# Kernel optimization log

Measured on AMD Instinct MI355X. Metric: run time of the kernel, lower is better.

The kernel has to match this reference:

```python
import jax, jax.numpy as jnp
import numpy as np

N = 50000      # nodes
E = 800000     # edges
IN = 256       # in_dim
HID = 64       # num_hidden
H0 = 4         # heads[0]
H1 = 1         # heads[1]
OUT1 = HID * H0  # 256, last GATConv out_feats
C = 64         # num_classes
NEG_SLOPE = 0.2


def setup_inputs() -> dict:
    ks = jax.random.split(jax.random.key(0), 13)
    s = 0.05
    return {
        "x":   jax.random.normal(ks[0], (N, IN), jnp.float32),
        "src": jax.random.randint(ks[1], (E,), 0, N, jnp.int32),
        "dst": jax.random.randint(ks[2], (E,), 0, N, jnp.int32),
        # layer 0: GATConv(IN, HID, H0)
        "W0":  jax.random.normal(ks[3], (IN, H0 * HID), jnp.float32) * s,
        "al0": jax.random.normal(ks[4], (H0, HID), jnp.float32) * s,
        "ar0": jax.random.normal(ks[5], (H0, HID), jnp.float32) * s,
        "b0":  jnp.zeros((H0 * HID,), jnp.float32),
        # layer 1: GATConv(H0*HID, OUT1, H1), residual (identity since in == H1*OUT1)
        "W1":  jax.random.normal(ks[6], (H0 * HID, H1 * OUT1), jnp.float32) * s,
        "al1": jax.random.normal(ks[7], (H1, OUT1), jnp.float32) * s,
        "ar1": jax.random.normal(ks[8], (H1, OUT1), jnp.float32) * s,
        "b1":  jnp.zeros((H1 * OUT1,), jnp.float32),
        # final classifier Linear(OUT1, C)
        "Wl":  jax.random.normal(ks[9], (OUT1, C), jnp.float32) * s,
        "bl":  jnp.zeros((C,), jnp.float32),
    }


def gat_conv(h, src, dst, W, al, ar, b, heads, out, residual, act):
    # ft: projected per-head features [N, H, D]
    ft = (h @ W).reshape(-1, heads, out)
    el = jnp.sum(ft * al, axis=-1)          # [N, H]
    er = jnp.sum(ft * ar, axis=-1)          # [N, H]
    e = jax.nn.leaky_relu(el[src] + er[dst], NEG_SLOPE)  # [E, H]
    # edge softmax grouped by destination node
    emax = jax.ops.segment_max(e, dst, num_segments=N)
    a = jnp.exp(e - emax[dst])
    asum = jax.ops.segment_sum(a, dst, num_segments=N)
    alpha = a / asum[dst]                   # [E, H]
    msg = alpha[:, :, None] * ft[src]       # [E, H, D]
    rst = jax.ops.segment_sum(msg, dst, num_segments=N)  # [N, H, D]
    if residual:  # identity residual (in_feats == heads*out)
        rst = rst + h.reshape(-1, heads, out)
    rst = rst + b.reshape(1, heads, out)
    if act is not None:
        rst = act(rst)
    return rst


def reference(x, src, dst, W0, al0, ar0, b0, W1, al1, ar1, b1, Wl, bl):
    h = gat_conv(x, src, dst, W0, al0, ar0, b0, H0, HID, False, jax.nn.elu)
    h = h.reshape(N, -1)                    # flatten(1) -> [N, H0*HID]
    h = gat_conv(h, src, dst, W1, al1, ar1, b1, H1, OUT1, True, None)
    h = h.mean(axis=1)                      # mean over heads -> [N, OUT1]
    logits = h @ Wl + bl
    return (logits, h)
```

## Files before the change

### kernel.cpp

```cpp
#include <hip/hip_runtime.h>
#include <hip/hip_bf16.h>
#include <stdint.h>

#define NNODES 50000
#define NEDGES 800000
#define CH     256
#define NCLS   64
#define DCAP   64

typedef __attribute__((ext_vector_type(8))) short  short8;
typedef __attribute__((ext_vector_type(4))) float  floatx4;

__device__ __forceinline__ float bf2f(unsigned short u) {
    union { unsigned int i; float f; } v; v.i = ((unsigned int)u) << 16; return v.f;
}
__device__ __forceinline__ unsigned short f2bf(float f) {
    union { float f; unsigned int i; } v; v.f = f;
    unsigned int x = v.i;
    return (unsigned short)((x + 0x7fffu + ((x >> 16) & 1u)) >> 16);
}

__device__ __forceinline__ void gl_lds16(const void* g, void* l) {
    __builtin_amdgcn_global_load_lds(
        (const __attribute__((address_space(1))) unsigned int*)g,
        (__attribute__((address_space(3))) unsigned int*)l, 16, 0, 0);
}

__global__ void k_setup(const float* __restrict__ W0, const float* __restrict__ W1,
                        const float* __restrict__ Wl, const float* __restrict__ x,
                        unsigned short* __restrict__ w0t, unsigned short* __restrict__ w1t,
                        unsigned short* __restrict__ wlt, unsigned short* __restrict__ xbf,
                        int* __restrict__ cnt) {
    int i = blockIdx.x * 256 + threadIdx.x;
    if (i < 65536) {
        int r = i >> 8, c = i & 255;
        w0t[c * 256 + r] = f2bf(W0[i]);
    } else if (i < 131072) {
        int j = i - 65536;
        int r = j >> 8, c = j & 255;
        w1t[c * 256 + r] = f2bf(W1[j]);
    } else if (i < 147456) {
        int j = i - 131072;
        int r = j >> 6, c = j & 63;
        wlt[c * 256 + r] = f2bf(Wl[j]);
    } else if (i < 147456 + NNODES) {
        cnt[i - 147456] = 0;
    } else {
        int j = i - (147456 + NNODES);
        if (j < NNODES * CH / 8) {
            const float4* xp = (const float4*)(x + (size_t)j * 8);
            float4 v0 = xp[0], v1 = xp[1];
            ushort4 o0, o1;
            o0.x = f2bf(v0.x); o0.y = f2bf(v0.y); o0.z = f2bf(v0.z); o0.w = f2bf(v0.w);
            o1.x = f2bf(v1.x); o1.y = f2bf(v1.y); o1.z = f2bf(v1.z); o1.w = f2bf(v1.w);
            *(ushort4*)(xbf + (size_t)j * 8)     = o0;
            *(ushort4*)(xbf + (size_t)j * 8 + 4) = o1;
        }
    }
}

__global__ void k_scatter(const int* __restrict__ dst, const int* __restrict__ src,
                          int* __restrict__ cnt, int* __restrict__ esrc) {
    int e = blockIdx.x * 256 + threadIdx.x;
    if (e < NEDGES) {
        int d = dst[e];
        if ((unsigned)d < NNODES) {
            int p = atomicAdd(&cnt[d], 1);
            if (p < DCAP) esrc[(size_t)d * DCAP + p] = src[e];
        }
    }
}

template<int BN, bool AF32, bool OUTF32, int HEL>
__global__ __launch_bounds__(256) void k_gemml(const void* __restrict__ Av,
                                               const unsigned short* __restrict__ BT,
                                               const float* __restrict__ bias,
                                               float* __restrict__ Cf,
                                               unsigned short* __restrict__ Cb,
                                               int M, int N,
                                               const float* __restrict__ al,
                                               const float* __restrict__ ar,
                                               float* __restrict__ el,
                                               float* __restrict__ er) {
    constexpr int NT  = BN / 16;
    constexpr int RPW = BN / 4;
    constexpr int P   = RPW / 16;
    __shared__ unsigned short Bs[2][BN][32];
    const int t  = threadIdx.x;
    const int w  = t >> 6, l = t & 63;
    const int lm = l & 15, lg = l >> 4;
    const int m0 = blockIdx.x * 64;
    const int arow = m0 + w * 16 + lm;
    const unsigned short* Ab = (const unsigned short*)Av;
    const float*          Af = (const float*)Av;

    const int srow  = w * RPW + (l >> 2);
    const int sslot = (l & 3) * 8;

    floatx4 acc[NT];
#pragma unroll
    for (int nt = 0; nt < NT; ++nt) acc[nt] = (floatx4)0.0f;

#pragma unroll
    for (int p = 0; p < P; ++p)
        gl_lds16(BT + (size_t)(srow + p * 16) * 256 + sslot,
                 &Bs[0][w * RPW + p * 16][0]);
    short8 af0 = (short8)0, af1 = (short8)0;
    if (arow < M) {
        if (AF32) {
            const float* ap = Af + (size_t)arow * 256 + lg * 8;
            float4 v0 = *(const float4*)(ap), v1 = *(const float4*)(ap + 4);
            af0[0] = (short)f2bf(v0.x); af0[1] = (short)f2bf(v0.y);
            af0[2] = (short)f2bf(v0.z); af0[3] = (short)f2bf(v0.w);
            af0[4] = (short)f2bf(v1.x); af0[5] = (short)f2bf(v1.y);
            af0[6] = (short)f2bf(v1.z); af0[7] = (short)f2bf(v1.w);
        } else {
            af0 = *(const short8*)(Ab + (size_t)arow * 256 + lg * 8);
        }
    }
    __syncthreads();

    int cur = 0;
    for (int ks = 0; ks < 8; ++ks) {
        if (ks < 7) {
            int k1 = (ks + 1) * 32;
#pragma unroll
            for (int p = 0; p < P; ++p)
                gl_lds16(BT + (size_t)(srow + p * 16) * 256 + k1 + sslot,
                         &Bs[cur ^ 1][w * RPW + p * 16][0]);
            af1 = (short8)0;
            if (arow < M) {
                if (AF32) {
                    const float* ap = Af + (size_t)arow * 256 + k1 + lg * 8;
                    float4 v0 = *(const float4*)(ap), v1 = *(const float4*)(ap + 4);
                    af1[0] = (short)f2bf(v0.x); af1[1] = (short)f2bf(v0.y);
                    af1[2] = (short)f2bf(v0.z); af1[3] = (short)f2bf(v0.w);
                    af1[4] = (short)f2bf(v1.x); af1[5] = (short)f2bf(v1.y);
                    af1[6] = (short)f2bf(v1.z); af1[7] = (short)f2bf(v1.w);
                } else {
                    af1 = *(const short8*)(Ab + (size_t)arow * 256 + k1 + lg * 8);
                }
            }
        }
#pragma unroll
        for (int nt = 0; nt < NT; ++nt) {
            short8 bf = *(const short8*)&Bs[cur][nt * 16 + lm][lg * 8];
            acc[nt] = __builtin_amdgcn_mfma_f32_16x16x32_bf16(af0, bf, acc[nt], 0, 0, 0);
        }
        af0 = af1;
        if (ks < 7) { __syncthreads(); cur ^= 1; }
    }

    float alv[HEL > 0 ? NT : 1], arv[HEL > 0 ? NT : 1];
    if (HEL > 0) {
#pragma unroll
        for (int nt = 0; nt < NT; ++nt) {
            alv[nt] = al[nt * 16 + lm];
            arv[nt] = ar[nt * 16 + lm];
        }
    }

#pragma unroll
    for (int j = 0; j < 4; ++j) {
        int row = m0 + w * 16 + (l >> 4) * 4 + j;
        if (row < M) {
#pragma unroll
            for (int nt = 0; nt < NT; ++nt) {
                int gcol = nt * 16 + lm;
                float v = acc[nt][j];
                if (bias) v += bias[gcol];
                if (OUTF32) Cf[(size_t)row * N + gcol] = v;
                else        Cb[(size_t)row * N + gcol] = f2bf(v);
            }
            if (HEL > 0) {
#pragma unroll
                for (int h = 0; h < HEL; ++h) {
                    float sl = 0.f, sr = 0.f;
#pragma unroll
                    for (int q = 0; q < NT / HEL; ++q) {
                        int nt = h * (NT / HEL) + q;
                        float v = acc[nt][j];
                        sl += v * alv[nt];
                        sr += v * arv[nt];
                    }
#pragma unroll
                    for (int mm = 1; mm < 16; mm <<= 1) {
                        sl += __shfl_xor(sl, mm, 64);
                        sr += __shfl_xor(sr, mm, 64);
                    }
                    if (lm == 0) {
                        el[(size_t)row * HEL + h] = sl;
                        er[(size_t)row * HEL + h] = sr;
                    }
                }
            }
        }
    }
}

template<int H, bool ELU, bool RESID>
__global__ __launch_bounds__(256) void k_agg5(
        const unsigned short* __restrict__ ft,
        const float* __restrict__ el, const float* __restrict__ er,
        const int* __restrict__ cnt,
        const int* __restrict__ esrc,
        const unsigned short* __restrict__ resid16,
        const float* __restrict__ bias,
        unsigned short* __restrict__ out_bf,
        float* __restrict__ out_f) {
    int w = threadIdx.x >> 6;
    int n = blockIdx.x * 4 + w;
    int l = threadIdx.x & 63;
    int c = 4 * l;
    int st = n * DCAP;
    int dg = __builtin_amdgcn_readfirstlane(cnt[n]);
    if (dg > DCAP) dg = DCAP;
    if (dg < 0) dg = 0;
    float a0 = 0.f, a1 = 0.f, a2 = 0.f, a3 = 0.f, wsum = 0.f;
    const unsigned short* ftc = ft + c;

    if (H == 1) {
        float ern = er[n];
        for (int i = 0; i < dg; i += 64) {
            int idx = i + l;
            int sv = 0; float wv = 0.f;
            if (idx < dg) {
                sv = esrc[st + idx];
                float xv = el[sv] + ern;
                xv = (xv > 0.f) ? xv : 0.2f * xv;
                xv = fminf(xv, 60.f);
                wv = __expf(xv);
            }
            wsum += wv;
            int jmax = dg - i; if (jmax > 64) jmax = 64;
            int j = 0;
            for (; j + 4 <= jmax; j += 4) {
                int s0 = __builtin_amdgcn_readlane(sv, j + 0);
                int s1 = __builtin_amdgcn_readlane(sv, j + 1);
                int s2 = __builtin_amdgcn_readlane(sv, j + 2);
                int s3 = __builtin_amdgcn_readlane(sv, j + 3);
                float w0 = __int_as_float(__builtin_amdgcn_readlane(__float_as_int(wv), j + 0));
                float w1 = __int_as_float(__builtin_amdgcn_readlane(__float_as_int(wv), j + 1));
                float w2 = __int_as_float(__builtin_amdgcn_readlane(__float_as_int(wv), j + 2));
                float w3 = __int_as_float(__builtin_amdgcn_readlane(__float_as_int(wv), j + 3));
                ushort4 f0 = *(const ushort4*)(ftc + (size_t)s0 * CH);
                ushort4 f1 = *(const ushort4*)(ftc + (size_t)s1 * CH);
                ushort4 f2 = *(const ushort4*)(ftc + (size_t)s2 * CH);
                ushort4 f3 = *(const ushort4*)(ftc + (size_t)s3 * CH);
                a0 += w0 * bf2f(f0.x) + w1 * bf2f(f1.x) + w2 * bf2f(f2.x) + w3 * bf2f(f3.x);
                a1 += w0 * bf2f(f0.y) + w1 * bf2f(f1.y) + w2 * bf2f(f2.y) + w3 * bf2f(f3.y);
                a2 += w0 * bf2f(f0.z) + w1 * bf2f(f1.z) + w2 * bf2f(f2.z) + w3 * bf2f(f3.z);
                a3 += w0 * bf2f(f0.w) + w1 * bf2f(f1.w) + w2 * bf2f(f2.w) + w3 * bf2f(f3.w);
            }
            for (; j < jmax; ++j) {
                int s0 = __builtin_amdgcn_readlane(sv, j);
                float w0 = __int_as_float(__builtin_amdgcn_readlane(__float_as_int(wv), j));
                ushort4 f0 = *(const ushort4*)(ftc + (size_t)s0 * CH);
                a0 += w0 * bf2f(f0.x); a1 += w0 * bf2f(f0.y);
                a2 += w0 * bf2f(f0.z); a3 += w0 * bf2f(f0.w);
            }
        }
#pragma unroll
        for (int m = 1; m < 64; m <<= 1) wsum += __shfl_xor(wsum, m, 64);
    } else {
        int head = l & 3, slot = l >> 2;
        int h = l >> 4;
        float ern = er[n * 4 + head];
        for (int i = 0; i < dg; i += 16) {
            int idx = i + slot;
            int sv = 0; float wv = 0.f;
            if (idx < dg) {
                sv = esrc[st + idx];
                float xv = el[sv * 4 + head] + ern;
                xv = (xv > 0.f) ? xv : 0.2f * xv;
                xv = fminf(xv, 60.f);
                wv = __expf(xv);
            }
            wsum += wv;
            int jmax = dg - i; if (jmax > 16) jmax = 16;
            int j = 0;
            for (; j + 4 <= jmax; j += 4) {
                int s0 = __builtin_amdgcn_readlane(sv, 4 * (j + 0));
                int s1 = __builtin_amdgcn_readlane(sv, 4 * (j + 1));
                int s2 = __builtin_amdgcn_readlane(sv, 4 * (j + 2));
                int s3 = __builtin_amdgcn_readlane(sv, 4 * (j + 3));
                float w0 = __shfl(wv, 4 * (j + 0) + h, 64);
                float w1 = __shfl(wv, 4 * (j + 1) + h, 64);
                float w2 = __shfl(wv, 4 * (j + 2) + h, 64);
                float w3 = __shfl(wv, 4 * (j + 3) + h, 64);
                ushort4 f0 = *(const ushort4*)(ftc + (size_t)s0 * CH);
                ushort4 f1 = *(const ushort4*)(ftc + (size_t)s1 * CH);
                ushort4 f2 = *(const ushort4*)(ftc + (size_t)s2 * CH);
                ushort4 f3 = *(const ushort4*)(ftc + (size_t)s3 * CH);
                a0 += w0 * bf2f(f0.x) + w1 * bf2f(f1.x) + w2 * bf2f(f2.x) + w3 * bf2f(f3.x);
                a1 += w0 * bf2f(f0.y) + w1 * bf2f(f1.y) + w2 * bf2f(f2.y) + w3 * bf2f(f3.y);
                a2 += w0 * bf2f(f0.z) + w1 * bf2f(f1.z) + w2 * bf2f(f2.z) + w3 * bf2f(f3.z);
                a3 += w0 * bf2f(f0.w) + w1 * bf2f(f1.w) + w2 * bf2f(f2.w) + w3 * bf2f(f3.w);
            }
            for (; j < jmax; ++j) {
                int s0 = __builtin_amdgcn_readlane(sv, 4 * j);
                float w0 = __shfl(wv, 4 * j + h, 64);
                ushort4 f0 = *(const ushort4*)(ftc + (size_t)s0 * CH);
                a0 += w0 * bf2f(f0.x); a1 += w0 * bf2f(f0.y);
                a2 += w0 * bf2f(f0.z); a3 += w0 * bf2f(f0.w);
            }
        }
#pragma unroll
        for (int m = 4; m < 64; m <<= 1) wsum += __shfl_xor(wsum, m, 64);
        wsum = __shfl(wsum, l >> 4, 64);
    }
    float inv = (wsum > 1e-30f) ? 1.0f / wsum : 0.0f;
    a0 *= inv; a1 *= inv; a2 *= inv; a3 *= inv;
    if (RESID) {
        ushort4 r = *(const ushort4*)(resid16 + (size_t)n * CH + c);
        a0 += bf2f(r.x); a1 += bf2f(r.y); a2 += bf2f(r.z); a3 += bf2f(r.w);
    }
    {
        float4 b = *(const float4*)(bias + c);
        a0 += b.x; a1 += b.y; a2 += b.z; a3 += b.w;
    }
    if (ELU) {
        a0 = (a0 > 0.f) ? a0 : __expf(a0) - 1.f;
        a1 = (a1 > 0.f) ? a1 : __expf(a1) - 1.f;
        a2 = (a2 > 0.f) ? a2 : __expf(a2) - 1.f;
        a3 = (a3 > 0.f) ? a3 : __expf(a3) - 1.f;
    }
    if (out_bf) {
        ushort4 ov; ov.x = f2bf(a0); ov.y = f2bf(a1); ov.z = f2bf(a2); ov.w = f2bf(a3);
        *(ushort4*)(out_bf + (size_t)n * CH + c) = ov;
    }
    if (out_f) {
        *(float4*)(out_f + (size_t)n * CH + c) = make_float4(a0, a1, a2, a3);
    }
}


extern "C" void kernel_launch(void* const* d_in, const int* in_sizes, int n_in,
                              void* d_out, int out_size, void* d_ws, size_t ws_size,
                              hipStream_t stream) {
    const float* x   = (const float*)d_in[0];
    const int*   src = (const int*)d_in[1];
    const int*   dst = (const int*)d_in[2];
    const float* W0  = (const float*)d_in[3];
    const float* al0 = (const float*)d_in[4];
    const float* ar0 = (const float*)d_in[5];
    const float* b0  = (const float*)d_in[6];
    const float* W1  = (const float*)d_in[7];
    const float* al1 = (const float*)d_in[8];
    const float* ar1 = (const float*)d_in[9];
    const float* b1  = (const float*)d_in[10];
    const float* Wl  = (const float*)d_in[11];
    const float* bl  = (const float*)d_in[12];

    float* out_logits = (float*)d_out;
    float* out_h      = out_logits + (size_t)NNODES * NCLS;

    unsigned short* xbf = (unsigned short*)out_h;

    char* ws = (char*)d_ws;
    size_t o = 0;
    auto alloc = [&](size_t b) { char* p = ws + o; o += (b + 255) & ~(size_t)255; return p; };
    unsigned short* ft   = (unsigned short*)alloc((size_t)NNODES * CH * 2);
    unsigned short* h0bf = (unsigned short*)alloc((size_t)NNODES * CH * 2);
    int*            esrc = (int*)alloc((size_t)NNODES * DCAP * 4);
    unsigned short* w0t  = (unsigned short*)alloc(256 * 256 * 2);
    unsigned short* w1t  = (unsigned short*)alloc(256 * 256 * 2);
    unsigned short* wlt  = (unsigned short*)alloc(64 * 256 * 2);
    int*            cnt  = (int*)alloc((size_t)NNODES * 4);
    float*          el0  = (float*)alloc((size_t)NNODES * 4 * 4);
    float*          er0  = (float*)alloc((size_t)NNODES * 4 * 4);
    float*          el1  = (float*)alloc((size_t)NNODES * 4);
    float*          er1  = (float*)alloc((size_t)NNODES * 4);

    int setup_items = 147456 + NNODES + NNODES * CH / 8;
    k_setup<<<(setup_items + 255) / 256, 256, 0, stream>>>(W0, W1, Wl, x,
                                                           w0t, w1t, wlt, xbf, cnt);
    k_scatter<<<(NEDGES + 255) / 256, 256, 0, stream>>>(dst, src, cnt, esrc);

    int gm = (NNODES + 63) / 64;
    k_gemml<256, false, false, 4><<<gm, 256, 0, stream>>>(
        xbf, w0t, nullptr, nullptr, ft, NNODES, CH, al0, ar0, el0, er0);
    k_agg5<4, true, false><<<NNODES / 4, 256, 0, stream>>>(
        ft, el0, er0, cnt, esrc, nullptr, b0, h0bf, nullptr);
    k_gemml<256, false, false, 1><<<gm, 256, 0, stream>>>(
        h0bf, w1t, nullptr, nullptr, ft, NNODES, CH, al1, ar1, el1, er1);
    k_agg5<1, false, true><<<NNODES / 4, 256, 0, stream>>>(
        ft, el1, er1, cnt, esrc, h0bf, b1, nullptr, out_h);
    k_gemml<64, true, true, 0><<<gm, 256, 0, stream>>>(
        out_h, wlt, bl, out_logits, nullptr, NNODES, NCLS,
        nullptr, nullptr, nullptr, nullptr);
}
```

Measured before the change: 355.2 us.

## Stage whole weight matrix in LDS with swizzle, 224-row blocks of 7 compute waves

Replaces the double-buffered K-loop GEMM with a kernel that loads the entire transposed weight matrix into shared memory once per block, using an XOR swizzle to avoid bank conflicts. Each of 7 active waves computes two 16-row tiles, so every B fragment read from LDS feeds two MFMAs. All A fragments are preloaded into registers. The aim is to cut per-K-step barriers and repeated weight staging across many small blocks. The cost is a 128KB LDS footprint, which limits occupancy to one block per CU, and an idle eighth wave used only for loading.

Result: faster. 345.0 us (-2.9%).

```diff
diff --git a/kernel.cpp b/kernel.cpp
--- a/kernel.cpp
+++ b/kernel.cpp
@@ -7,6 +7,7 @@
 #define CH     256
 #define NCLS   64
 #define DCAP   64
+#define RB     224
 
 typedef __attribute__((ext_vector_type(8))) short  short8;
 typedef __attribute__((ext_vector_type(4))) float  floatx4;
@@ -72,83 +73,82 @@
 }
 
 template<int BN, bool AF32, bool OUTF32, int HEL>
-__global__ __launch_bounds__(256) void k_gemml(const void* __restrict__ Av,
-                                               const unsigned short* __restrict__ BT,
-                                               const float* __restrict__ bias,
-                                               float* __restrict__ Cf,
-                                               unsigned short* __restrict__ Cb,
-                                               int M, int N,
-                                               const float* __restrict__ al,
-                                               const float* __restrict__ ar,
-                                               float* __restrict__ el,
-                                               float* __restrict__ er) {
-    constexpr int NT  = BN / 16;
-    constexpr int RPW = BN / 4;
-    constexpr int P   = RPW / 16;
-    __shared__ unsigned short Bs[2][BN][32];
+__global__ __launch_bounds__(512, 1) void k_gemmw(
+        const void* __restrict__ Av, const unsigned short* __restrict__ BT,
+        const float* __restrict__ bias,
+        float* __restrict__ Cf, unsigned short* __restrict__ Cb,
+        int M, int N,
+        const float* __restrict__ al, const float* __restrict__ ar,
+        float* __restrict__ el, float* __restrict__ er) {
+    constexpr int NT     = BN / 16;
+    constexpr int ROUNDS = (BN * 512) / 8192;
+    __shared__ unsigned short Bw[BN * 256];
     const int t  = threadIdx.x;
     const int w  = t >> 6, l = t & 63;
     const int lm = l & 15, lg = l >> 4;
-    const int m0 = blockIdx.x * 64;
-    const int arow = m0 + w * 16 + lm;
+
+#pragma unroll
+    for (int r = 0; r < ROUNDS; ++r) {
+        int g   = r * 8192 + t * 16;
+        int row = g >> 9;
+        int bir = g & 511;
+        int sb  = (g & ~511) | (bir ^ ((row & 7) << 4));
+        gl_lds16((const char*)BT + sb, (char*)Bw + r * 8192 + w * 1024);
+    }
+
+    const int m0    = blockIdx.x * RB;
+    const int Mb    = (m0 + RB < M) ? (m0 + RB) : M;
+    const int tile0 = m0 + w * 32;
+    const bool active = (w < 7) && (tile0 < Mb);
+
     const unsigned short* Ab = (const unsigned short*)Av;
     const float*          Af = (const float*)Av;
-
-    const int srow  = w * RPW + (l >> 2);
-    const int sslot = (l & 3) * 8;
-
-    floatx4 acc[NT];
-#pragma unroll
-    for (int nt = 0; nt < NT; ++nt) acc[nt] = (floatx4)0.0f;
-
-#pragma unroll
-    for (int p = 0; p < P; ++p)
-        gl_lds16(BT + (size_t)(srow + p * 16) * 256 + sslot,
-                 &Bs[0][w * RPW + p * 16][0]);
-    short8 af0 = (short8)0, af1 = (short8)0;
-    if (arow < M) {
-        if (AF32) {
-            const float* ap = Af + (size_t)arow * 256 + lg * 8;
-            float4 v0 = *(const float4*)(ap), v1 = *(const float4*)(ap + 4);
-            af0[0] = (short)f2bf(v0.x); af0[1] = (short)f2bf(v0.y);
-            af0[2] = (short)f2bf(v0.z); af0[3] = (short)f2bf(v0.w);
-            af0[4] = (short)f2bf(v1.x); af0[5] = (short)f2bf(v1.y);
-            af0[6] = (short)f2bf(v1.z); af0[7] = (short)f2bf(v1.w);
-        } else {
-            af0 = *(const short8*)(Ab + (size_t)arow * 256 + lg * 8);
-        }
-    }
+    short8 af[2][8];
+#pragma unroll
+    for (int g = 0; g < 2; ++g) {
+        int arow = tile0 + g * 16 + lm;
+        bool ok = active && (arow < M);
+#pragma unroll
+        for (int ks = 0; ks < 8; ++ks) {
+            if (AF32) {
+                short8 v = (short8)0;
+                if (ok) {
+                    const float* ap = Af + (size_t)arow * 256 + ks * 32 + lg * 8;
+                    float4 v0 = *(const float4*)(ap), v1 = *(const float4*)(ap + 4);
+                    v[0] = (short)f2bf(v0.x); v[1] = (short)f2bf(v0.y);
+                    v[2] = (short)f2bf(v0.z); v[3] = (short)f2bf(v0.w);
+                    v[4] = (short)f2bf(v1.x); v[5] = (short)f2bf(v1.y);
+                    v[6] = (short)f2bf(v1.z); v[7] = (short)f2bf(v1.w);
+                }
+                af[g][ks] = v;
+            } else {
+                af[g][ks] = ok ? *(const short8*)(Ab + (size_t)arow * 256 + ks * 32 + lg * 8)
+                               : (short8)0;
+            }
+        }
+    }
+
     __syncthreads();
-
-    int cur = 0;
+    if (!active) return;
+
+    floatx4 acc[2][NT];
+#pragma unroll
+    for (int g = 0; g < 2; ++g)
+#pragma unroll
+        for (int nt = 0; nt < NT; ++nt) acc[g][nt] = (floatx4)0.0f;
+
+    const int kx   = (lm >> 2) & 1;
+    const int coff = (lg * 16) ^ ((lm & 3) << 4);
+    const char* Bb = (const char*)Bw;
+#pragma unroll
     for (int ks = 0; ks < 8; ++ks) {
-        if (ks < 7) {
-            int k1 = (ks + 1) * 32;
-#pragma unroll
-            for (int p = 0; p < P; ++p)
-                gl_lds16(BT + (size_t)(srow + p * 16) * 256 + k1 + sslot,
-                         &Bs[cur ^ 1][w * RPW + p * 16][0]);
-            af1 = (short8)0;
-            if (arow < M) {
-                if (AF32) {
-                    const float* ap = Af + (size_t)arow * 256 + k1 + lg * 8;
-                    float4 v0 = *(const float4*)(ap), v1 = *(const float4*)(ap + 4);
-                    af1[0] = (short)f2bf(v0.x); af1[1] = (short)f2bf(v0.y);
-                    af1[2] = (short)f2bf(v0.z); af1[3] = (short)f2bf(v0.w);
-                    af1[4] = (short)f2bf(v1.x); af1[5] = (short)f2bf(v1.y);
-                    af1[6] = (short)f2bf(v1.z); af1[7] = (short)f2bf(v1.w);
-                } else {
-                    af1 = *(const short8*)(Ab + (size_t)arow * 256 + k1 + lg * 8);
-                }
-            }
-        }
+        int kk = (ks ^ kx) * 64;
 #pragma unroll
         for (int nt = 0; nt < NT; ++nt) {
-            short8 bf = *(const short8*)&Bs[cur][nt * 16 + lm][lg * 8];
-            acc[nt] = __builtin_amdgcn_mfma_f32_16x16x32_bf16(af0, bf, acc[nt], 0, 0, 0);
-        }
-        af0 = af1;
-        if (ks < 7) { __syncthreads(); cur ^= 1; }
+            short8 bf = *(const short8*)(Bb + (nt * 16 + lm) * 512 + kk + coff);
+            acc[0][nt] = __builtin_amdgcn_mfma_f32_16x16x32_bf16(af[0][ks], bf, acc[0][nt], 0, 0, 0);
+            acc[1][nt] = __builtin_amdgcn_mfma_f32_16x16x32_bf16(af[1][ks], bf, acc[1][nt], 0, 0, 0);
+        }
     }
 
     float alv[HEL > 0 ? NT : 1], arv[HEL > 0 ? NT : 1];
@@ -159,43 +159,44 @@
             arv[nt] = ar[nt * 16 + lm];
         }
     }
-
-#pragma unroll
-    for (int j = 0; j < 4; ++j) {
-        int row = m0 + w * 16 + (l >> 4) * 4 + j;
-        if (row < M) {
-#pragma unroll
-            for (int nt = 0; nt < NT; ++nt) {
-                int gcol = nt * 16 + lm;
-                float v = acc[nt][j];
-                if (bias) v += bias[gcol];
-                if (OUTF32) Cf[(size_t)row * N + gcol] = v;
-                else        Cb[(size_t)row * N + gcol] = f2bf(v);
-            }
-            if (HEL > 0) {
-#pragma unroll
-                for (int h = 0; h < HEL; ++h) {
-                    float sl = 0.f, sr = 0.f;
-#pragma unroll
-                    for (int q = 0; q < NT / HEL; ++q) {
-                        int nt = h * (NT / HEL) + q;
-                        float v = acc[nt][j];
-                        sl += v * alv[nt];
-                        sr += v * arv[nt];
-                    }
-#pragma unroll
-                    for (int mm = 1; mm < 16; mm <<= 1) {
-                        sl += __shfl_xor(sl, mm, 64);
-                        sr += __shfl_xor(sr, mm, 64);
-                    }
-                    if (lm == 0) {
-                        el[(size_t)row * HEL + h] = sl;
-                        er[(size_t)row * HEL + h] = sr;
+#pragma unroll
+    for (int g = 0; g < 2; ++g)
+#pragma unroll
+        for (int j = 0; j < 4; ++j) {
+            int row = tile0 + g * 16 + lg * 4 + j;
+            if (row < Mb) {
+#pragma unroll
+                for (int nt = 0; nt < NT; ++nt) {
+                    int gcol = nt * 16 + lm;
+                    float v = acc[g][nt][j];
+                    if (bias) v += bias[gcol];
+                    if (OUTF32) Cf[(size_t)row * N + gcol] = v;
+                    else        Cb[(size_t)row * N + gcol] = f2bf(v);
+                }
+                if (HEL > 0) {
+#pragma unroll
+                    for (int h = 0; h < HEL; ++h) {
+                        float sl = 0.f, sr = 0.f;
+#pragma unroll
+                        for (int q = 0; q < NT / HEL; ++q) {
+                            int nt = h * (NT / HEL) + q;
+                            float v = acc[g][nt][j];
+                            sl += v * alv[nt];
+                            sr += v * arv[nt];
+                        }
+#pragma unroll
+                        for (int mm = 1; mm < 16; mm <<= 1) {
+                            sl += __shfl_xor(sl, mm, 64);
+                            sr += __shfl_xor(sr, mm, 64);
+                        }
+                        if (lm == 0) {
+                            el[(size_t)row * HEL + h] = sl;
+                            er[(size_t)row * HEL + h] = sr;
+                        }
                     }
                 }
             }
         }
-    }
 }
 
 template<int H, bool ELU, bool RESID>
@@ -377,16 +378,16 @@
                                                            w0t, w1t, wlt, xbf, cnt);
     k_scatter<<<(NEDGES + 255) / 256, 256, 0, stream>>>(dst, src, cnt, esrc);
 
-    int gm = (NNODES + 63) / 64;
-    k_gemml<256, false, false, 4><<<gm, 256, 0, stream>>>(
+    int gm = (NNODES + RB - 1) / RB;
+    k_gemmw<256, false, false, 4><<<gm, 512, 0, stream>>>(
         xbf, w0t, nullptr, nullptr, ft, NNODES, CH, al0, ar0, el0, er0);
     k_agg5<4, true, false><<<NNODES / 4, 256, 0, stream>>>(
         ft, el0, er0, cnt, esrc, nullptr, b0, h0bf, nullptr);
-    k_gemml<256, false, false, 1><<<gm, 256, 0, stream>>>(
+    k_gemmw<256, false, false, 1><<<gm, 512, 0, stream>>>(
         h0bf, w1t, nullptr, nullptr, ft, NNODES, CH, al1, ar1, el1, er1);
     k_agg5<1, false, true><<<NNODES / 4, 256, 0, stream>>>(
         ft, el1, er1, cnt, esrc, h0bf, b1, nullptr, out_h);
-    k_gemml<64, true, true, 0><<<gm, 256, 0, stream>>>(
+    k_gemmw<64, true, true, 0><<<gm, 512, 0, stream>>>(
         out_h, wlt, bl, out_logits, nullptr, NNODES, NCLS,
         nullptr, nullptr, nullptr, nullptr);
 }
```
